# Kernel tuning notes

Hardware: AMD Instinct MI355X
Metric: run time of the kernel (lower is better)

## Reference

```python
import jax, jax.numpy as jnp
import numpy as np

EPS = 1e-5

def _dwconv1d(x, w):
    # x: [B,C,L], w: [C,k] depthwise kernel, same padding, no bias
    k = w.shape[1]
    return jax.lax.conv_general_dilated(
        x, w[:, None, :], window_strides=(1,), padding=[(k // 2, k // 2)],
        dimension_numbers=('NCH', 'OIH', 'NCH'), feature_group_count=x.shape[1])

def _bn1d(x, gamma, beta, mean, var):
    # eval-mode BatchNorm over channel dim of [B,C,L]
    scale = gamma / jnp.sqrt(var + EPS)
    return (x - mean[:, None]) * scale[:, None] + beta[:, None]

def _strip_pool(x, w3, w7, gamma, beta, mean, var):
    # mean of [identity, dwconv_k3, dwconv_k7] then BN
    out = (x + _dwconv1d(x, w3) + _dwconv1d(x, w7)) / 3.0
    return _bn1d(out, gamma, beta, mean, var)

def _hswish(x):
    return x * jnp.clip(x + 3.0, 0.0, 6.0) / 6.0

def setup_inputs() -> dict:
    key = jax.random.key(0)
    ks = jax.random.split(key, 8)
    B, C, H, W = 32, 256, 64, 64   # C = 2*inp
    MIP = 8                        # max(8, 128//32)
    O = 256                        # 2*oup
    f32 = jnp.float32
    x = jax.random.normal(ks[0], (B, C, H, W), f32)
    def bn_params(k, n):
        k1, k2 = jax.random.split(k)
        return (1.0 + 0.1 * jax.random.normal(k1, (n,), f32),      # gamma
                0.1 * jax.random.normal(k2, (n,), f32),            # beta
                jnp.zeros((n,), f32),                              # running_mean
                jnp.ones((n,), f32))                               # running_var
    sph_g, sph_b, sph_m, sph_v = bn_params(ks[1], C)
    spw_g, spw_b, spw_m, spw_v = bn_params(ks[2], C)
    bn1_g, bn1_b, bn1_m, bn1_v = bn_params(ks[3], MIP)
    s = 0.1
    return {
        'x': x,
        'sph_w3': s * jax.random.normal(ks[4], (C, 3), f32),
        'sph_w7': s * jax.random.normal(ks[4], (C, 7), f32),
        'sph_gamma': sph_g, 'sph_beta': sph_b, 'sph_mean': sph_m, 'sph_var': sph_v,
        'spw_w3': s * jax.random.normal(ks[5], (C, 3), f32),
        'spw_w7': s * jax.random.normal(ks[5], (C, 7), f32),
        'spw_gamma': spw_g, 'spw_beta': spw_b, 'spw_mean': spw_m, 'spw_var': spw_v,
        'conv1_w': s * jax.random.normal(ks[6], (MIP, C), f32),
        'bn1_gamma': bn1_g, 'bn1_beta': bn1_b, 'bn1_mean': bn1_m, 'bn1_var': bn1_v,
        'convh_w': s * jax.random.normal(ks[7], (O, MIP), f32),
        'convw_w': s * jax.random.normal(ks[7], (O, MIP), f32),
    }

def reference(x, sph_w3, sph_w7, sph_gamma, sph_beta, sph_mean, sph_var,
              spw_w3, spw_w7, spw_gamma, spw_beta, spw_mean, spw_var,
              conv1_w, bn1_gamma, bn1_beta, bn1_mean, bn1_var,
              convh_w, convw_w):
    B, C, H, W = x.shape
    # coordinate pooling -> strips [B,C,H] and [B,C,W]
    x_h = jnp.mean(x, axis=3)
    x_w = jnp.mean(x, axis=2)
    # multi-scale strip pooling
    x_h = _strip_pool(x_h, sph_w3, sph_w7, sph_gamma, sph_beta, sph_mean, sph_var)
    x_w = _strip_pool(x_w, spw_w3, spw_w7, spw_gamma, spw_beta, spw_mean, spw_var)
    # shared 1x1 conv + BN + h_swish on concatenated strip [B,C,H+W]
    y = jnp.concatenate([x_h, x_w], axis=2)
    y = jnp.einsum('mc,bcl->bml', conv1_w, y)
    y = _bn1d(y, bn1_gamma, bn1_beta, bn1_mean, bn1_var)
    y = _hswish(y)
    y_h, y_w = y[:, :, :H], y[:, :, H:]
    # per-direction gates [B,O,H] / [B,O,W]
    a_h = jax.nn.sigmoid(jnp.einsum('om,bmh->boh', convh_w, y_h))
    a_w = jax.nn.sigmoid(jnp.einsum('om,bmw->bow', convw_w, y_w))
    return x * a_h[:, :, :, None] * a_w[:, :, None, :]
```

## Files before the change

kernel.cpp:

```cpp
#include <hip/hip_runtime.h>
#include <math.h>

#define EPSF 1e-5f

typedef float float4v __attribute__((ext_vector_type(4)));

__global__ __launch_bounds__(256) void k1_pool_strip(
    const float* __restrict__ x,
    const float* __restrict__ sph_w3, const float* __restrict__ sph_w7,
    const float* __restrict__ sph_g,  const float* __restrict__ sph_b,
    const float* __restrict__ sph_m,  const float* __restrict__ sph_v,
    const float* __restrict__ spw_w3, const float* __restrict__ spw_w7,
    const float* __restrict__ spw_g,  const float* __restrict__ spw_b,
    const float* __restrict__ spw_m,  const float* __restrict__ spw_v,
    float* __restrict__ sp)
{
    __shared__ __align__(16) float tile[64][68];
    __shared__ __align__(16) float rpart[256];
    __shared__ float cpart[4][64];
    __shared__ float mh[64];
    __shared__ float mw[64];

    const int plane = blockIdx.x;
    const int c = plane & 255;
    const float* xp = x + (size_t)plane * 4096;
    const int t = threadIdx.x;
    const int r = t >> 2, q = t & 3;

    const float4* src = (const float4*)(xp + r * 64 + q * 16);
    float4 v0 = src[0], v1 = src[1], v2 = src[2], v3 = src[3];
    float4* dst = (float4*)&tile[r][q * 16];
    dst[0] = v0; dst[1] = v1; dst[2] = v2; dst[3] = v3;
    rpart[t] = (v0.x + v0.y + v0.z + v0.w) + (v1.x + v1.y + v1.z + v1.w)
             + (v2.x + v2.y + v2.z + v2.w) + (v3.x + v3.y + v3.z + v3.w);
    __syncthreads();

    {
        const int cc = t & 63, qw = t >> 6;
        float s = 0.f;
        #pragma unroll
        for (int i = 0; i < 16; ++i) s += tile[qw * 16 + i][cc];
        cpart[qw][cc] = s;
    }
    __syncthreads();

    if (t < 64) {
        float4 rp = ((const float4*)rpart)[t];
        mh[t] = (rp.x + rp.y + rp.z + rp.w) * (1.f / 64.f);
        mw[t] = (cpart[0][t] + cpart[1][t] + cpart[2][t] + cpart[3][t]) * (1.f / 64.f);
    }
    __syncthreads();

    if (t < 128) {
        const int l = t & 63;
        const bool is_h = (t < 64);
        const float* m  = is_h ? mh     : mw;
        const float* w3 = is_h ? sph_w3 : spw_w3;
        const float* w7 = is_h ? sph_w7 : spw_w7;
        const float* g  = is_h ? sph_g  : spw_g;
        const float* bb = is_h ? sph_b  : spw_b;
        const float* mu = is_h ? sph_m  : spw_m;
        const float* vv = is_h ? sph_v  : spw_v;

        float v[7];
        #pragma unroll
        for (int j = 0; j < 7; ++j) {
            int idx = l - 3 + j;
            v[j] = (idx >= 0 && idx < 64) ? m[idx] : 0.f;
        }
        float c3 = w3[c*3+0]*v[2] + w3[c*3+1]*v[3] + w3[c*3+2]*v[4];
        float c7 = 0.f;
        #pragma unroll
        for (int j = 0; j < 7; ++j) c7 += w7[c*7+j]*v[j];

        float o = (v[3] + c3 + c7) * (1.f / 3.f);
        float scale = g[c] * rsqrtf(vv[c] + EPSF);
        o = (o - mu[c]) * scale + bb[c];
        sp[(size_t)plane * 128 + (is_h ? l : 64 + l)] = o;
    }
}

__global__ __launch_bounds__(256) void k2_mid(
    const float* __restrict__ sp,
    const float* __restrict__ conv1_w,
    const float* __restrict__ bn1_g, const float* __restrict__ bn1_b,
    const float* __restrict__ bn1_m, const float* __restrict__ bn1_v,
    const float* __restrict__ convh_w, const float* __restrict__ convw_w,
    float* __restrict__ a_h, float* __restrict__ a_w)
{
    __shared__ float spc[256 * 16];
    __shared__ float w1t[256 * 8];
    __shared__ float wos[256 * 8];
    __shared__ float ys[8 * 16];

    const int b  = blockIdx.x >> 3;
    const int lc = blockIdx.x & 7;
    const int l0 = lc * 16;
    const bool is_h = (l0 < 64);
    const int t = threadIdx.x;

    const float* spb = sp + (size_t)b * 256 * 128;
    const float* wo  = is_h ? convh_w : convw_w;

    for (int j = t; j < 4096; j += 256) {
        int cc = j >> 4, li = j & 15;
        spc[j] = spb[cc * 128 + l0 + li];
    }
    for (int j = t; j < 2048; j += 256) {
        int cc = j >> 3, m = j & 7;
        w1t[j] = conv1_w[m * 256 + cc];
        wos[j] = wo[j];
    }
    __syncthreads();

    if (t < 128) {
        const int m = t >> 4, li = t & 15;
        float acc = 0.f;
        for (int cc = 0; cc < 256; ++cc)
            acc += w1t[cc * 8 + m] * spc[cc * 16 + li];
        float scale = bn1_g[m] * rsqrtf(bn1_v[m] + EPSF);
        float val = (acc - bn1_m[m]) * scale + bn1_b[m];
        val = val * fminf(fmaxf(val + 3.f, 0.f), 6.f) * (1.f / 6.f);
        ys[m * 16 + li] = val;
    }
    __syncthreads();

    float* ab = (is_h ? a_h : a_w) + (size_t)b * 256 * 64;
    const int pos0 = is_h ? l0 : l0 - 64;
    const int li = t & 15, ob = t >> 4;
    #pragma unroll
    for (int i = 0; i < 16; ++i) {
        const int o = i * 16 + ob;
        float s = 0.f;
        #pragma unroll
        for (int m = 0; m < 8; ++m)
            s += wos[o * 8 + m] * ys[m * 16 + li];
        ab[o * 64 + pos0 + li] = 1.f / (1.f + __expf(-s));
    }
}

__global__ __launch_bounds__(256) void k3_apply(
    const float* __restrict__ x,
    const float* __restrict__ a_h, const float* __restrict__ a_w,
    float* __restrict__ out)
{
    const size_t g = (size_t)blockIdx.x * 256 + threadIdx.x;
    float4 xv = ((const float4*)x)[g];
    const size_t idx = g * 4;
    const int w0 = (int)(idx & 63);
    const int h  = (int)((idx >> 6) & 63);
    const size_t bc = idx >> 12;
    const float ah = a_h[bc * 64 + h];
    const float4 aw = *(const float4*)(a_w + bc * 64 + w0);
    float4v o;
    o.x = xv.x * ah * aw.x;
    o.y = xv.y * ah * aw.y;
    o.z = xv.z * ah * aw.z;
    o.w = xv.w * ah * aw.w;
    __builtin_nontemporal_store(o, (float4v*)out + g);
}

extern "C" void kernel_launch(void* const* d_in, const int* in_sizes, int n_in,
                              void* d_out, int out_size, void* d_ws, size_t ws_size,
                              hipStream_t stream) {
    const float* x       = (const float*)d_in[0];
    const float* sph_w3  = (const float*)d_in[1];
    const float* sph_w7  = (const float*)d_in[2];
    const float* sph_g   = (const float*)d_in[3];
    const float* sph_b   = (const float*)d_in[4];
    const float* sph_m   = (const float*)d_in[5];
    const float* sph_v   = (const float*)d_in[6];
    const float* spw_w3  = (const float*)d_in[7];
    const float* spw_w7  = (const float*)d_in[8];
    const float* spw_g   = (const float*)d_in[9];
    const float* spw_b   = (const float*)d_in[10];
    const float* spw_m   = (const float*)d_in[11];
    const float* spw_v   = (const float*)d_in[12];
    const float* conv1_w = (const float*)d_in[13];
    const float* bn1_g   = (const float*)d_in[14];
    const float* bn1_b   = (const float*)d_in[15];
    const float* bn1_m   = (const float*)d_in[16];
    const float* bn1_v   = (const float*)d_in[17];
    const float* convh_w = (const float*)d_in[18];
    const float* convw_w = (const float*)d_in[19];

    float* ws  = (float*)d_ws;
    float* sp  = ws;
    float* a_h = ws + 1048576;
    float* a_w = ws + 1048576 + 524288;

    const int B = 32, C = 256;

    k1_pool_strip<<<B * C, 256, 0, stream>>>(
        x, sph_w3, sph_w7, sph_g, sph_b, sph_m, sph_v,
        spw_w3, spw_w7, spw_g, spw_b, spw_m, spw_v, sp);

    k2_mid<<<B * 8, 256, 0, stream>>>(
        sp, conv1_w, bn1_g, bn1_b, bn1_m, bn1_v, convh_w, convw_w, a_h, a_w);

    k3_apply<<<32768, 256, 0, stream>>>(x, a_h, a_w, (float*)d_out);
}
```

Baseline: 292.6 us.

## Fuse gate projection and sigmoid into per-plane apply kernel

The 8-to-256 gate projection and sigmoid move out of the middle kernel and into the apply kernel, which now runs one block per (b,c) plane. Each block loads the shared y strip for its batch, computes its 128 gate values into shared memory, then scales the plane's 4096 elements with them. This drops the a_h/a_w workspace round trip and the per-element gather of gate values, at the cost of two syncs and a small redundant y load in every plane block.

```diff
diff --git a/kernel.cpp b/kernel.cpp
--- a/kernel.cpp
+++ b/kernel.cpp
@@ -80,27 +80,22 @@
     }
 }
 
-__global__ __launch_bounds__(256) void k2_mid(
+__global__ __launch_bounds__(256) void k2_y(
     const float* __restrict__ sp,
     const float* __restrict__ conv1_w,
     const float* __restrict__ bn1_g, const float* __restrict__ bn1_b,
     const float* __restrict__ bn1_m, const float* __restrict__ bn1_v,
-    const float* __restrict__ convh_w, const float* __restrict__ convw_w,
-    float* __restrict__ a_h, float* __restrict__ a_w)
+    float* __restrict__ y)
 {
     __shared__ float spc[256 * 16];
     __shared__ float w1t[256 * 8];
-    __shared__ float wos[256 * 8];
-    __shared__ float ys[8 * 16];
 
     const int b  = blockIdx.x >> 3;
     const int lc = blockIdx.x & 7;
     const int l0 = lc * 16;
-    const bool is_h = (l0 < 64);
     const int t = threadIdx.x;
 
     const float* spb = sp + (size_t)b * 256 * 128;
-    const float* wo  = is_h ? convh_w : convw_w;
 
     for (int j = t; j < 4096; j += 256) {
         int cc = j >> 4, li = j & 15;
@@ -109,7 +104,6 @@
     for (int j = t; j < 2048; j += 256) {
         int cc = j >> 3, m = j & 7;
         w1t[j] = conv1_w[m * 256 + cc];
-        wos[j] = wo[j];
     }
     __syncthreads();
 
@@ -121,43 +115,63 @@
         float scale = bn1_g[m] * rsqrtf(bn1_v[m] + EPSF);
         float val = (acc - bn1_m[m]) * scale + bn1_b[m];
         val = val * fminf(fmaxf(val + 3.f, 0.f), 6.f) * (1.f / 6.f);
-        ys[m * 16 + li] = val;
-    }
-    __syncthreads();
-
-    float* ab = (is_h ? a_h : a_w) + (size_t)b * 256 * 64;
-    const int pos0 = is_h ? l0 : l0 - 64;
-    const int li = t & 15, ob = t >> 4;
-    #pragma unroll
-    for (int i = 0; i < 16; ++i) {
-        const int o = i * 16 + ob;
-        float s = 0.f;
-        #pragma unroll
-        for (int m = 0; m < 8; ++m)
-            s += wos[o * 8 + m] * ys[m * 16 + li];
-        ab[o * 64 + pos0 + li] = 1.f / (1.f + __expf(-s));
+        y[(size_t)b * 1024 + m * 128 + l0 + li] = val;
     }
 }
 
 __global__ __launch_bounds__(256) void k3_apply(
     const float* __restrict__ x,
-    const float* __restrict__ a_h, const float* __restrict__ a_w,
+    const float* __restrict__ y,
+    const float* __restrict__ convh_w, const float* __restrict__ convw_w,
     float* __restrict__ out)
 {
-    const size_t g = (size_t)blockIdx.x * 256 + threadIdx.x;
-    float4 xv = ((const float4*)x)[g];
-    const size_t idx = g * 4;
-    const int w0 = (int)(idx & 63);
-    const int h  = (int)((idx >> 6) & 63);
-    const size_t bc = idx >> 12;
-    const float ah = a_h[bc * 64 + h];
-    const float4 aw = *(const float4*)(a_w + bc * 64 + w0);
-    float4v o;
-    o.x = xv.x * ah * aw.x;
-    o.y = xv.y * ah * aw.y;
-    o.z = xv.z * ah * aw.z;
-    o.w = xv.w * ah * aw.w;
-    __builtin_nontemporal_store(o, (float4v*)out + g);
+    __shared__ float ys[8 * 128];
+    __shared__ float att[128];
+
+    const int plane = blockIdx.x;
+    const int b = plane >> 8, c = plane & 255;
+    const int t = threadIdx.x;
+
+    const float* xp = x + (size_t)plane * 4096;
+    float* op = out + (size_t)plane * 4096;
+
+    float4 xv0 = ((const float4*)xp)[t];
+    float4 xv1 = ((const float4*)xp)[t + 256];
+    float4 xv2 = ((const float4*)xp)[t + 512];
+    float4 xv3 = ((const float4*)xp)[t + 768];
+
+    const float* yb = y + (size_t)b * 1024;
+    for (int j = t; j < 1024; j += 256) ys[j] = yb[j];
+    __syncthreads();
+
+    if (t < 128) {
+        const bool is_h = (t < 64);
+        const int l = t & 63;
+        const float* wo = (is_h ? convh_w : convw_w) + c * 8;
+        const float* yrow = ys + (is_h ? l : 64 + l);
+        float s = 0.f;
+        #pragma unroll
+        for (int m = 0; m < 8; ++m)
+            s += wo[m] * yrow[m * 128];
+        att[t] = 1.f / (1.f + __expf(-s));
+    }
+    __syncthreads();
+
+    #pragma unroll
+    for (int k = 0; k < 4; ++k) {
+        const int g = k * 256 + t;
+        const int h = g >> 4;
+        const int w0 = (g & 15) * 4;
+        const float4 xv = (k == 0) ? xv0 : (k == 1) ? xv1 : (k == 2) ? xv2 : xv3;
+        const float ah = att[h];
+        const float4 aw = *(const float4*)&att[64 + w0];
+        float4v o;
+        o.x = xv.x * ah * aw.x;
+        o.y = xv.y * ah * aw.y;
+        o.z = xv.z * ah * aw.z;
+        o.w = xv.w * ah * aw.w;
+        __builtin_nontemporal_store(o, (float4v*)op + g);
+    }
 }
 
 extern "C" void kernel_launch(void* const* d_in, const int* in_sizes, int n_in,
@@ -184,10 +198,9 @@
     const float* convh_w = (const float*)d_in[18];
     const float* convw_w = (const float*)d_in[19];
 
-    float* ws  = (float*)d_ws;
-    float* sp  = ws;
-    float* a_h = ws + 1048576;
-    float* a_w = ws + 1048576 + 524288;
+    float* ws = (float*)d_ws;
+    float* sp = ws;
+    float* yy = ws + 1048576;
 
     const int B = 32, C = 256;
 
@@ -195,8 +208,8 @@
         x, sph_w3, sph_w7, sph_g, sph_b, sph_m, sph_v,
         spw_w3, spw_w7, spw_g, spw_b, spw_m, spw_v, sp);
 
-    k2_mid<<<B * 8, 256, 0, stream>>>(
-        sp, conv1_w, bn1_g, bn1_b, bn1_m, bn1_v, convh_w, convw_w, a_h, a_w);
-
-    k3_apply<<<32768, 256, 0, stream>>>(x, a_h, a_w, (float*)d_out);
-}
+    k2_y<<<B * 8, 256, 0, stream>>>(
+        sp, conv1_w, bn1_g, bn1_b, bn1_m, bn1_v, yy);
+
+    k3_apply<<<B * C, 256, 0, stream>>>(x, yy, convh_w, convw_w, (float*)d_out);
+}
```

After: 296.8 us. Within noise of the previous version (+1.4%).
